# Kernel optimization log

Measured on AMD Instinct MI355X. Metric: run time of the kernel, lower is better.

The kernel has to match this reference:

```python
import jax, jax.numpy as jnp
import numpy as np
from jax import lax

N_QUBITS = 4
DIM = 2 ** N_QUBITS  # 16, amplitude-embedding feature size == clayer_in output
N_QLAYERS = 1
INPUT_SIZE = 128
HIDDEN_SIZE = 128
BATCH = 128
SEQ = 1024


def _cnot_perm(n):
    # Composed permutation matrix of the ansatz CNOT ladder:
    # for i in 1..2: for j in range(n): CNOT(wire j -> wire (j+i) % n)
    # PennyLane wire ordering: wire 0 is the most significant bit.
    dim = 2 ** n
    gates = []
    for i in range(1, 3):
        for j in range(n):
            gates.append((j, (j + i) % n))
    P = np.eye(dim, dtype=np.float32)
    for (c, t) in gates:
        cbit, tbit = n - 1 - c, n - 1 - t
        g = np.zeros((dim, dim), dtype=np.float32)
        for s in range(dim):
            s2 = s ^ (1 << tbit) if (s >> cbit) & 1 else s
            g[s2, s] = 1.0
        P = g @ P  # psi_new = P @ psi
    return P

_P = jnp.asarray(_cnot_perm(N_QUBITS))
# Z[s, w] = <s| PauliZ(wire w) |s>
_Z = jnp.asarray(np.array([[1.0 - 2.0 * ((s >> (N_QUBITS - 1 - w)) & 1)
                            for w in range(N_QUBITS)] for s in range(DIM)],
                           dtype=np.float32))


def _rx_kron(theta):
    # kron of per-wire RX(theta_i) gates, wire 0 most significant
    c = jnp.cos(theta / 2).astype(jnp.complex64)
    s = (-1j * jnp.sin(theta / 2)).astype(jnp.complex64)
    u = None
    for i in range(N_QUBITS):
        m = jnp.stack([jnp.stack([c[i], s[i]]), jnp.stack([s[i], c[i]])])
        u = m if u is None else jnp.kron(u, m)
    return u  # (DIM, DIM) complex64


def _vqc(y, weights):
    # AmplitudeEmbedding(normalize=True) + n_qlayers x (CNOT ladder, RX layer)
    # then expval(PauliZ) on each wire. y: (B, DIM) real, weights: (L, V, n)
    norm = jnp.sqrt(jnp.sum(y * y, axis=1, keepdims=True))
    psi = (y / norm).astype(jnp.complex64)  # (B, DIM)
    for l in range(N_QLAYERS):
        psi = psi @ _P.T               # CNOT ladder (permutation)
        psi = psi @ _rx_kron(weights[l, 0]).T  # RX layer (only vrotation 0 used)
    probs = (psi * jnp.conj(psi)).real
    return probs @ _Z  # (B, n_qubits)


def _cell(h, x_t, w_r, w_r1, w_u, W_in, b_in, W_out, b_out):
    y = jnp.concatenate([h, x_t], axis=1) @ W_in + b_in
    r = jax.nn.sigmoid(_vqc(y, w_r) @ W_out + b_out)
    v1 = jnp.concatenate([r * h, x_t], axis=1) @ W_in + b_in
    h2 = jnp.tanh(_vqc(v1, w_r1) @ W_out + b_out)
    z = jax.nn.sigmoid(_vqc(y, w_u) @ W_out + b_out)
    return (1.0 - z) * h + z * h2


def _run(xs, w_r, w_r1, w_u, W_in, b_in, W_out, b_out):
    # xs: (T, B, F); returns hidden states in loop order, shape (B, T, H)
    h0 = jnp.zeros((xs.shape[1], HIDDEN_SIZE), dtype=xs.dtype)
    def step(h, x_t):
        hn = _cell(h, x_t, w_r, w_r1, w_u, W_in, b_in, W_out, b_out)
        return hn, hn
    _, hs = lax.scan(step, h0, xs)
    return jnp.swapaxes(hs, 0, 1)


def setup_inputs() -> dict:
    key = jax.random.key(0)
    ks = jax.random.split(key, 11)
    concat = INPUT_SIZE + HIDDEN_SIZE
    two_pi = 2.0 * float(np.pi)
    return {
        "x": jax.random.normal(ks[0], (BATCH, SEQ, INPUT_SIZE), jnp.float32),
        "W_in": jax.random.normal(ks[1], (concat, DIM), jnp.float32) / np.float32(np.sqrt(concat)),
        "b_in": jax.random.normal(ks[2], (DIM,), jnp.float32) * 0.01,
        "W_out": jax.random.normal(ks[3], (N_QUBITS, HIDDEN_SIZE), jnp.float32) / np.float32(np.sqrt(N_QUBITS)),
        "b_out": jax.random.normal(ks[4], (HIDDEN_SIZE,), jnp.float32) * 0.01,
        "w_reset": jax.random.uniform(ks[5], (N_QLAYERS, 1, N_QUBITS), jnp.float32, 0.0, two_pi),
        "w_reset1": jax.random.uniform(ks[6], (N_QLAYERS, 1, N_QUBITS), jnp.float32, 0.0, two_pi),
        "w_update": jax.random.uniform(ks[7], (N_QLAYERS, 1, N_QUBITS), jnp.float32, 0.0, two_pi),
        "w_back_reset": jax.random.uniform(ks[8], (N_QLAYERS, 1, N_QUBITS), jnp.float32, 0.0, two_pi),
        "w_back_reset1": jax.random.uniform(ks[9], (N_QLAYERS, 1, N_QUBITS), jnp.float32, 0.0, two_pi),
        "w_back_update": jax.random.uniform(ks[10], (N_QLAYERS, 1, N_QUBITS), jnp.float32, 0.0, two_pi),
    }


def reference(x, W_in, b_in, W_out, b_out, w_reset, w_reset1, w_update,
              w_back_reset, w_back_reset1, w_back_update):
    xs = jnp.swapaxes(x, 0, 1)  # (T, B, F)
    fwd = _run(xs, w_reset, w_reset1, w_update, W_in, b_in, W_out, b_out)
    # Original backward loop iterates t = T-1..0 and stacks in loop order,
    # then adds WITHOUT flipping back. Reproduce that exactly.
    bwd = _run(xs[::-1], w_back_reset, w_back_reset1, w_back_update,
               W_in, b_in, W_out, b_out)
    return (fwd + bwd) / 2.0
```

## Files before the change

kernel.cpp:

```cpp
#include <hip/hip_runtime.h>
#include <hip/hip_bf16.h>

#define TSEQ 1024
#define NB   128
#define HID  128
#define QDIM 16

typedef unsigned int  u32;
typedef unsigned short u16;
typedef float f32x2 __attribute__((ext_vector_type(2)));


template<int CTRL>
__device__ __forceinline__ int dpp_i(int x) {
  return __builtin_amdgcn_update_dpp(0, x, CTRL, 0xF, 0xF, true);
}
template<int CTRL>
__device__ __forceinline__ float dpp_f(float x) {
  return __int_as_float(dpp_i<CTRL>(__float_as_int(x)));
}

#ifdef __has_builtin
#if __has_builtin(__builtin_amdgcn_permlane16_swap) && __has_builtin(__builtin_amdgcn_permlane32_swap)
#define HAS_PLS 1
#endif
#endif
#ifndef HAS_PLS
#define HAS_PLS 0
#endif

__device__ __forceinline__ float pls16_sum(float x) {
#if HAS_PLS
  auto r = __builtin_amdgcn_permlane16_swap(__float_as_uint(x), __float_as_uint(x), false, false);
  return __uint_as_float(r[0]) + __uint_as_float(r[1]);
#else
  return x + __shfl_xor(x, 16, 64);
#endif
}
__device__ __forceinline__ float pls32_sum(float x) {
#if HAS_PLS
  auto r = __builtin_amdgcn_permlane32_swap(__float_as_uint(x), __float_as_uint(x), false, false);
  return __uint_as_float(r[0]) + __uint_as_float(r[1]);
#else
  return x + __shfl_xor(x, 32, 64);
#endif
}

__device__ __forceinline__ float rcpf(float x) { return __builtin_amdgcn_rcpf(x); }

__device__ __forceinline__ float ex2(float x) {
#if defined(__has_builtin)
#if __has_builtin(__builtin_amdgcn_exp2f)
  return __builtin_amdgcn_exp2f(x);
#else
  return exp2f(x);
#endif
#else
  return exp2f(x);
#endif
}

__device__ __forceinline__ u16 f2bf(float f) {
  u32 u = __float_as_uint(f);
  u32 r = (u + 0x7FFFu + ((u >> 16) & 1u)) >> 16;
  return (u16)r;
}

__device__ __forceinline__ f32x2 s2(float x) { f32x2 r; r.x = x; r.y = x; return r; }

__device__ __forceinline__ int gperm(int t) {
  int u = t;
#define APPLY(c, tt) u ^= (((u >> (3 - (c))) & 1) << (3 - (tt)));
  APPLY(3, 1) APPLY(2, 0) APPLY(1, 3) APPLY(0, 2)
  APPLY(3, 0) APPLY(2, 3) APPLY(1, 2) APPLY(0, 1)
#undef APPLY
  return u;
}


__global__ __launch_bounds__(256) void xw_kernel(
    const float* __restrict__ x, const float* __restrict__ W_in,
    const float* __restrict__ b_in, float* __restrict__ xw) {
  __shared__ __align__(16) float xs[16][132];
  __shared__ float wl[2048];
  __shared__ float bl[16];
  const int tid = threadIdx.x;
  const long r0 = (long)blockIdx.x * 16;
#pragma unroll
  for (int i = 0; i < 8; ++i) {
    int idx = tid + i * 256;
    xs[idx >> 7][idx & 127] = x[(r0 + (idx >> 7)) * 128 + (idx & 127)];
  }
#pragma unroll
  for (int i = 0; i < 8; ++i) {
    int idx = tid + i * 256;
    wl[idx] = W_in[2048 + idx];
  }
  if (tid < 16) bl[tid] = b_in[tid];
  __syncthreads();
  const int rr = tid >> 4, j = tid & 15;
  const int gj = gperm(j);
  float s = bl[gj];
#pragma unroll
  for (int k4 = 0; k4 < 32; ++k4) {
    float4 v = *reinterpret_cast<const float4*>(&xs[rr][k4 * 4]);
    int kb = k4 * 4;
    s = fmaf(v.x, wl[(kb + 0) * 16 + gj], s);
    s = fmaf(v.y, wl[(kb + 1) * 16 + gj], s);
    s = fmaf(v.z, wl[(kb + 2) * 16 + gj], s);
    s = fmaf(v.w, wl[(kb + 3) * 16 + gj], s);
  }
  xw[(r0 + rr) * 16 + j] = s;
}


template<bool BF16WS>
__global__ __launch_bounds__(64)
__attribute__((amdgpu_waves_per_eu(1, 2)))
void qbigru_main(
    const float* __restrict__ W_in,
    const float* __restrict__ W_out,
    const float* __restrict__ b_out,
    const float* __restrict__ thr_f, const float* __restrict__ thr1_f, const float* __restrict__ thu_f,
    const float* __restrict__ thr_b, const float* __restrict__ thr1_b, const float* __restrict__ thu_b,
    const float* __restrict__ xw,
    float* __restrict__ out,
    void* __restrict__ bwdws) {
  const int tid = threadIdx.x;
  const int l4  = tid & 15;
  const int dir = blockIdx.x >> 7;
  const int b   = blockIdx.x & 127;

  const int pshl = dpp_i<0x104>(tid);
  const int sel4 = (pshl == (tid ^ 4)) ? ~0 : 0;
  auto xor4f = [&](float x) {
    int a = dpp_i<0x104>(__float_as_int(x));
    int c = dpp_i<0x114>(__float_as_int(x));
    return __int_as_float((a & sel4) | (c & ~sel4));
  };

  auto bfr = [&](const float* v) -> float {
    float w1[8];
#pragma unroll
    for (int j = 0; j < 8; ++j) w1[j] = v[2 * j] + dpp_f<0xB1>(v[2 * j + 1]);
    float w2[4];
#pragma unroll
    for (int j = 0; j < 4; ++j) w2[j] = w1[2 * j] + dpp_f<0x4E>(w1[2 * j + 1]);
    float w3[2];
#pragma unroll
    for (int j = 0; j < 2; ++j) w3[j] = w2[j] + dpp_f<0x128>(w2[j + 2]);
    float y0 = w3[0] + xor4f(w3[1]);
    return pls32_sum(pls16_sum(y0));
  };

  auto ebf = [&](float p, float& n2, float* eb) {
    float s4 = xor4f(p);
    float P  = p + s4, M2 = p - s4;
    float dP = dpp_f<0x128>(P), dM2 = dpp_f<0x128>(M2);
    float P3 = P + dP, M3 = P - dP; M2 = M2 + dM2;
    float a1 = dpp_f<0x4E>(P3), a2 = dpp_f<0x4E>(M3), a3 = dpp_f<0x4E>(M2);
    float P1 = P3 + a1, M1 = P3 - a1; M3 += a2; M2 += a3;
    float b0_ = dpp_f<0xB1>(P1), b1_ = dpp_f<0xB1>(M1), b3_ = dpp_f<0xB1>(M3), b2_ = dpp_f<0xB1>(M2);
    n2 = P1 + b0_;
    eb[0] = P1 - b0_; eb[1] = M1 + b1_; eb[3] = M3 + b3_; eb[2] = M2 + b2_;
  };

  const float* thr  = dir ? thr_b  : thr_f;
  const float* thr1 = dir ? thr1_b : thr1_f;
  const float* thu  = dir ? thu_b  : thu_f;

  const int k0 = 2 * tid, k1 = 2 * tid + 1;

  f32x2 w0p[8], w1p[8];
#pragma unroll
  for (int i = 0; i < 8; ++i) {
    int ja = gperm((2 * i) ^ l4), jb = gperm((2 * i + 1) ^ l4);
    f32x2 a, c;
    a.x = W_in[k0 * QDIM + ja];  a.y = W_in[k0 * QDIM + jb];
    c.x = W_in[k1 * QDIM + ja];  c.y = W_in[k1 * QDIM + jb];
    w0p[i] = a; w1p[i] = c;
  }

  const float L2E = 1.4426950408889634f;
  f32x2 woRpk[4], woZpk[4], woHpk[4];
#pragma unroll
  for (int B = 0; B < 4; ++B) {
    float sgn = ((tid >> B) & 1) ? -1.f : 1.f;
    float cR = cosf(thr[3 - B])  * sgn * (-L2E);
    float cZ = cosf(thu[3 - B])  * sgn * (-L2E);
    float cH = cosf(thr1[3 - B]) * sgn * (2.f * L2E);
    float wo0 = W_out[(3 - B) * HID + k0];
    float wo1 = W_out[(3 - B) * HID + k1];
    f32x2 rr_, zz_, hh_;
    rr_.x = wo0 * cR;  rr_.y = wo1 * cR;
    zz_.x = wo0 * cZ;  zz_.y = wo1 * cZ;
    hh_.x = wo0 * cH;  hh_.y = wo1 * cH;
    woRpk[B] = rr_; woZpk[B] = zz_; woHpk[B] = hh_;
  }
  f32x2 nbcpk, bc2pk;
  nbcpk.x = -b_out[k0] * L2E;         nbcpk.y = -b_out[k1] * L2E;
  bc2pk.x =  b_out[k0] * (2.f * L2E); bc2pk.y =  b_out[k1] * (2.f * L2E);

  auto dot4pk = [](const float* e, const f32x2* w) -> f32x2 {
    f32x2 d01 = s2(e[1]) * w[1] + s2(e[0]) * w[0];
    f32x2 d23 = s2(e[3]) * w[3] + s2(e[2]) * w[2];
    return d01 + d23;
  };

  f32x2 hpk; hpk.x = 0.f; hpk.y = 0.f;
  const float* pxw = xw + ((long)b * TSEQ + (dir ? TSEQ - 1 : 0)) * QDIM;
  const long xstep = dir ? -QDIM : QDIM;
  float xc = pxw[l4]; pxw += xstep;
  float xn = pxw[l4]; pxw += xstep;

  float* po  = out + (long)b * TSEQ * HID + k0;
  float* pbf = (float*)bwdws + (long)b * TSEQ * HID + k0;
  u32*   pbh = (u32*)bwdws + ((long)b * TSEQ * HID >> 1) + tid;

#pragma unroll 1
  for (int t = 0; t < TSEQ; ++t) {
    float xnn = pxw[l4]; pxw += xstep;

    f32x2 hh0 = s2(hpk.x);
    f32x2 hh1 = s2(hpk.y);
    float v[16];
#pragma unroll
    for (int i = 0; i < 8; ++i) {
      f32x2 a = hh0 * w0p[i] + hh1 * w1p[i];
      v[2 * i] = a.x; v[2 * i + 1] = a.y;
    }
    float yv = bfr(v) + xc;

    float prb = yv * yv;

    float n2, eb[4];
    ebf(prb, n2, eb);
    float inv = rcpf(n2);

    f32x2 rd = dot4pk(eb, woRpk);
    f32x2 zd = dot4pk(eb, woZpk);

    f32x2 ra = rd * s2(inv) + nbcpk;
    f32x2 za = zd * s2(inv) + nbcpk;
    float r0 = rcpf(1.f + ex2(ra.x));
    float r1 = rcpf(1.f + ex2(ra.y));
    float z0 = rcpf(1.f + ex2(za.x));
    float z1 = rcpf(1.f + ex2(za.y));

    f32x2 zpk;  zpk.x = z0; zpk.y = z1;
    f32x2 omz = s2(1.f) - zpk;
    f32x2 qpk = omz * hpk + zpk;
    f32x2 spk = s2(-2.f) * zpk;

    f32x2 rpk; rpk.x = r0; rpk.y = r1;
    f32x2 rh = rpk * hpk;
    hh0 = s2(rh.x);
    hh1 = s2(rh.y);
#pragma unroll
    for (int i = 0; i < 8; ++i) {
      f32x2 a = hh0 * w0p[i] + hh1 * w1p[i];
      v[2 * i] = a.x; v[2 * i + 1] = a.y;
    }
    float vv = bfr(v) + xc;

    float prb2 = vv * vv;

    float n2b, eb2[4];
    ebf(prb2, n2b, eb2);
    float invb = rcpf(n2b);
    f32x2 hd = dot4pk(eb2, woHpk);
    f32x2 ha = hd * s2(invb) + bc2pk;
    float wq0 = rcpf(1.f + ex2(ha.x));
    float wq1 = rcpf(1.f + ex2(ha.y));
    f32x2 wpk; wpk.x = wq0; wpk.y = wq1;
    hpk = spk * wpk + qpk;

    f32x2 opk = hpk * s2(0.5f);
    if (dir == 0) {
      *reinterpret_cast<f32x2*>(po) = opk;
      po += HID;
    } else if (BF16WS) {
      *pbh = (u32)f2bf(opk.x) | ((u32)f2bf(opk.y) << 16);
      pbh += HID / 2;
    } else {
      *reinterpret_cast<f32x2*>(pbf) = opk;
      pbf += HID;
    }

    xc = xn; xn = xnn;
  }
}


template<bool BF16WS>
__global__ __launch_bounds__(256) void combine_k(float* __restrict__ out,
                                                 const void* __restrict__ bwd, long n4) {
  long i = (long)blockIdx.x * 256 + threadIdx.x;
  const long stride = (long)gridDim.x * 256;
  for (; i < n4; i += stride) {
    float4 o = reinterpret_cast<float4*>(out)[i];
    float ax, ay, az, aw;
    if (BF16WS) {
      ushort4 u = reinterpret_cast<const ushort4*>(bwd)[i];
      ax = __uint_as_float((u32)u.x << 16);
      ay = __uint_as_float((u32)u.y << 16);
      az = __uint_as_float((u32)u.z << 16);
      aw = __uint_as_float((u32)u.w << 16);
    } else {
      float4 a = reinterpret_cast<const float4*>(bwd)[i];
      ax = a.x; ay = a.y; az = a.z; aw = a.w;
    }
    o.x += ax; o.y += ay; o.z += az; o.w += aw;
    reinterpret_cast<float4*>(out)[i] = o;
  }
}


extern "C" void kernel_launch(void* const* d_in, const int* in_sizes, int n_in,
                              void* d_out, int out_size, void* d_ws, size_t ws_size,
                              hipStream_t stream) {
  const float* x     = (const float*)d_in[0];
  const float* W_in  = (const float*)d_in[1];
  const float* b_in  = (const float*)d_in[2];
  const float* W_out = (const float*)d_in[3];
  const float* b_out = (const float*)d_in[4];
  const float* thr_f  = (const float*)d_in[5];
  const float* thr1_f = (const float*)d_in[6];
  const float* thu_f  = (const float*)d_in[7];
  const float* thr_b  = (const float*)d_in[8];
  const float* thr1_b = (const float*)d_in[9];
  const float* thu_b  = (const float*)d_in[10];
  float* out = (float*)d_out;

  char* ws = (char*)d_ws;
  const size_t PAD = 4096;
  const size_t xw_bytes = (size_t)NB * TSEQ * QDIM * sizeof(float);
  float* xw = (float*)(ws + PAD);
  void* bwd = (void*)(ws + PAD + xw_bytes + PAD);
  const size_t need_f32 = 2 * PAD + xw_bytes + (size_t)NB * TSEQ * HID * sizeof(float);
  const bool f32ws = (ws_size >= need_f32);

  xw_kernel<<<(NB * TSEQ) / 16, 256, 0, stream>>>(x, W_in, b_in, xw);

  if (f32ws) {
    qbigru_main<false><<<256, 64, 0, stream>>>(W_in, W_out, b_out,
        thr_f, thr1_f, thu_f, thr_b, thr1_b, thu_b, xw, out, bwd);
  } else {
    qbigru_main<true><<<256, 64, 0, stream>>>(W_in, W_out, b_out,
        thr_f, thr1_f, thu_f, thr_b, thr1_b, thu_b, xw, out, bwd);
  }

  const long n4 = (long)NB * TSEQ * HID / 4;
  if (f32ws) combine_k<false><<<2048, 256, 0, stream>>>(out, bwd, n4);
  else       combine_k<true><<<2048, 256, 0, stream>>>(out, bwd, n4);
}
```

Before: 590.8 us.

## Use row-rotate DPP butterfly reduction and always store backward output as bf16

Reworks the per-step 16-lane reduction to use DPP row-rotate patterns instead of xor swizzles, rotating the W_in weight assignment so each lane's partial products line up. A runtime probe of the rotate direction selects a specialized loop body. This removes the emulated xor-4 exchange (two DPP ops plus select) from the latency-critical recurrence. It also drops the fp32 backward workspace path and always writes bf16, halving workspace traffic at the cost of precision.

```diff
diff --git a/kernel.cpp b/kernel.cpp
--- a/kernel.cpp
+++ b/kernel.cpp
@@ -1,5 +1,6 @@
 #include <hip/hip_runtime.h>
 #include <hip/hip_bf16.h>
+#include <type_traits>
 
 #define TSEQ 1024
 #define NB   128
@@ -114,7 +115,6 @@
 }
 
 
-template<bool BF16WS>
 __global__ __launch_bounds__(64)
 __attribute__((amdgpu_waves_per_eu(1, 2)))
 void qbigru_main(
@@ -139,19 +139,8 @@
     return __int_as_float((a & sel4) | (c & ~sel4));
   };
 
-  auto bfr = [&](const float* v) -> float {
-    float w1[8];
-#pragma unroll
-    for (int j = 0; j < 8; ++j) w1[j] = v[2 * j] + dpp_f<0xB1>(v[2 * j + 1]);
-    float w2[4];
-#pragma unroll
-    for (int j = 0; j < 4; ++j) w2[j] = w1[2 * j] + dpp_f<0x4E>(w1[2 * j + 1]);
-    float w3[2];
-#pragma unroll
-    for (int j = 0; j < 2; ++j) w3[j] = w2[j] + dpp_f<0x128>(w2[j + 2]);
-    float y0 = w3[0] + xor4f(w3[1]);
-    return pls32_sum(pls16_sum(y0));
-  };
+  const int q1 = dpp_i<0x121>(l4);
+  const bool dplus = (q1 == ((l4 + 1) & 15));
 
   auto ebf = [&](float p, float& n2, float* eb) {
     float s4 = xor4f(p);
@@ -174,7 +163,7 @@
   f32x2 w0p[8], w1p[8];
 #pragma unroll
   for (int i = 0; i < 8; ++i) {
-    int ja = gperm((2 * i) ^ l4), jb = gperm((2 * i + 1) ^ l4);
+    int ja = gperm((2 * i + l4) & 15), jb = gperm((2 * i + 1 + l4) & 15);
     f32x2 a, c;
     a.x = W_in[k0 * QDIM + ja];  a.y = W_in[k0 * QDIM + jb];
     c.x = W_in[k1 * QDIM + ja];  c.y = W_in[k1 * QDIM + jb];
@@ -207,110 +196,122 @@
     return d01 + d23;
   };
 
-  f32x2 hpk; hpk.x = 0.f; hpk.y = 0.f;
-  const float* pxw = xw + ((long)b * TSEQ + (dir ? TSEQ - 1 : 0)) * QDIM;
-  const long xstep = dir ? -QDIM : QDIM;
-  float xc = pxw[l4]; pxw += xstep;
-  float xn = pxw[l4]; pxw += xstep;
-
-  float* po  = out + (long)b * TSEQ * HID + k0;
-  float* pbf = (float*)bwdws + (long)b * TSEQ * HID + k0;
-  u32*   pbh = (u32*)bwdws + ((long)b * TSEQ * HID >> 1) + tid;
+  auto body = [&](auto dpc) {
+    constexpr bool DP = decltype(dpc)::value;
+    constexpr int C2 = DP ? 0x12C : 0x124;
+    constexpr int C3 = DP ? 0x12E : 0x122;
+    constexpr int C4 = DP ? 0x12F : 0x121;
+
+    auto bfr = [&](const float* v) -> float {
+      float w1[8];
+#pragma unroll
+      for (int j = 0; j < 8; ++j) w1[j] = v[j] + dpp_f<0x128>(v[j + 8]);
+      float w2[4];
+#pragma unroll
+      for (int j = 0; j < 4; ++j) w2[j] = w1[j] + dpp_f<C2>(w1[j + 4]);
+      float w3[2];
+#pragma unroll
+      for (int j = 0; j < 2; ++j) w3[j] = w2[j] + dpp_f<C3>(w2[j + 2]);
+      float y0 = w3[0] + dpp_f<C4>(w3[1]);
+      return pls32_sum(pls16_sum(y0));
+    };
+
+    f32x2 hpk; hpk.x = 0.f; hpk.y = 0.f;
+    const float* pxw = xw + ((long)b * TSEQ + (dir ? TSEQ - 1 : 0)) * QDIM;
+    const long xstep = dir ? -QDIM : QDIM;
+    float xc = pxw[l4]; pxw += xstep;
+    float xn = pxw[l4]; pxw += xstep;
+
+    float* po  = out + (long)b * TSEQ * HID + k0;
+    u32*   pbh = (u32*)bwdws + ((long)b * TSEQ * HID >> 1) + tid;
 
 #pragma unroll 1
-  for (int t = 0; t < TSEQ; ++t) {
-    float xnn = pxw[l4]; pxw += xstep;
-
-    f32x2 hh0 = s2(hpk.x);
-    f32x2 hh1 = s2(hpk.y);
-    float v[16];
-#pragma unroll
-    for (int i = 0; i < 8; ++i) {
-      f32x2 a = hh0 * w0p[i] + hh1 * w1p[i];
-      v[2 * i] = a.x; v[2 * i + 1] = a.y;
+    for (int t = 0; t < TSEQ; ++t) {
+      float xnn = pxw[l4]; pxw += xstep;
+
+      f32x2 hh0 = s2(hpk.x);
+      f32x2 hh1 = s2(hpk.y);
+      float v[16];
+#pragma unroll
+      for (int i = 0; i < 8; ++i) {
+        f32x2 a = hh0 * w0p[i] + hh1 * w1p[i];
+        v[2 * i] = a.x; v[2 * i + 1] = a.y;
+      }
+      float yv = bfr(v) + xc;
+
+      float prb = yv * yv;
+
+      float n2, eb[4];
+      ebf(prb, n2, eb);
+      float inv = rcpf(n2);
+
+      f32x2 rd = dot4pk(eb, woRpk);
+      f32x2 zd = dot4pk(eb, woZpk);
+
+      f32x2 ra = rd * s2(inv) + nbcpk;
+      f32x2 za = zd * s2(inv) + nbcpk;
+      float r0 = rcpf(1.f + ex2(ra.x));
+      float r1 = rcpf(1.f + ex2(ra.y));
+      float z0 = rcpf(1.f + ex2(za.x));
+      float z1 = rcpf(1.f + ex2(za.y));
+
+      f32x2 zpk;  zpk.x = z0; zpk.y = z1;
+      f32x2 omz = s2(1.f) - zpk;
+      f32x2 qpk = omz * hpk + zpk;
+      f32x2 spk = s2(-2.f) * zpk;
+
+      f32x2 rpk; rpk.x = r0; rpk.y = r1;
+      f32x2 rh = rpk * hpk;
+      hh0 = s2(rh.x);
+      hh1 = s2(rh.y);
+#pragma unroll
+      for (int i = 0; i < 8; ++i) {
+        f32x2 a = hh0 * w0p[i] + hh1 * w1p[i];
+        v[2 * i] = a.x; v[2 * i + 1] = a.y;
+      }
+      float vv = bfr(v) + xc;
+
+      float prb2 = vv * vv;
+
+      float n2b, eb2[4];
+      ebf(prb2, n2b, eb2);
+      float invb = rcpf(n2b);
+      f32x2 hd = dot4pk(eb2, woHpk);
+      f32x2 ha = hd * s2(invb) + bc2pk;
+      float wq0 = rcpf(1.f + ex2(ha.x));
+      float wq1 = rcpf(1.f + ex2(ha.y));
+      f32x2 wpk; wpk.x = wq0; wpk.y = wq1;
+      hpk = spk * wpk + qpk;
+
+      f32x2 opk = hpk * s2(0.5f);
+      if (dir == 0) {
+        *reinterpret_cast<f32x2*>(po) = opk;
+        po += HID;
+      } else {
+        *pbh = (u32)f2bf(opk.x) | ((u32)f2bf(opk.y) << 16);
+        pbh += HID / 2;
+      }
+
+      xc = xn; xn = xnn;
     }
-    float yv = bfr(v) + xc;
-
-    float prb = yv * yv;
-
-    float n2, eb[4];
-    ebf(prb, n2, eb);
-    float inv = rcpf(n2);
-
-    f32x2 rd = dot4pk(eb, woRpk);
-    f32x2 zd = dot4pk(eb, woZpk);
-
-    f32x2 ra = rd * s2(inv) + nbcpk;
-    f32x2 za = zd * s2(inv) + nbcpk;
-    float r0 = rcpf(1.f + ex2(ra.x));
-    float r1 = rcpf(1.f + ex2(ra.y));
-    float z0 = rcpf(1.f + ex2(za.x));
-    float z1 = rcpf(1.f + ex2(za.y));
-
-    f32x2 zpk;  zpk.x = z0; zpk.y = z1;
-    f32x2 omz = s2(1.f) - zpk;
-    f32x2 qpk = omz * hpk + zpk;
-    f32x2 spk = s2(-2.f) * zpk;
-
-    f32x2 rpk; rpk.x = r0; rpk.y = r1;
-    f32x2 rh = rpk * hpk;
-    hh0 = s2(rh.x);
-    hh1 = s2(rh.y);
-#pragma unroll
-    for (int i = 0; i < 8; ++i) {
-      f32x2 a = hh0 * w0p[i] + hh1 * w1p[i];
-      v[2 * i] = a.x; v[2 * i + 1] = a.y;
-    }
-    float vv = bfr(v) + xc;
-
-    float prb2 = vv * vv;
-
-    float n2b, eb2[4];
-    ebf(prb2, n2b, eb2);
-    float invb = rcpf(n2b);
-    f32x2 hd = dot4pk(eb2, woHpk);
-    f32x2 ha = hd * s2(invb) + bc2pk;
-    float wq0 = rcpf(1.f + ex2(ha.x));
-    float wq1 = rcpf(1.f + ex2(ha.y));
-    f32x2 wpk; wpk.x = wq0; wpk.y = wq1;
-    hpk = spk * wpk + qpk;
-
-    f32x2 opk = hpk * s2(0.5f);
-    if (dir == 0) {
-      *reinterpret_cast<f32x2*>(po) = opk;
-      po += HID;
-    } else if (BF16WS) {
-      *pbh = (u32)f2bf(opk.x) | ((u32)f2bf(opk.y) << 16);
-      pbh += HID / 2;
-    } else {
-      *reinterpret_cast<f32x2*>(pbf) = opk;
-      pbf += HID;
-    }
-
-    xc = xn; xn = xnn;
-  }
-}
-
-
-template<bool BF16WS>
+  };
+
+  if (dplus) body(std::integral_constant<bool, true>{});
+  else       body(std::integral_constant<bool, false>{});
+}
+
+
 __global__ __launch_bounds__(256) void combine_k(float* __restrict__ out,
                                                  const void* __restrict__ bwd, long n4) {
   long i = (long)blockIdx.x * 256 + threadIdx.x;
   const long stride = (long)gridDim.x * 256;
   for (; i < n4; i += stride) {
     float4 o = reinterpret_cast<float4*>(out)[i];
-    float ax, ay, az, aw;
-    if (BF16WS) {
-      ushort4 u = reinterpret_cast<const ushort4*>(bwd)[i];
-      ax = __uint_as_float((u32)u.x << 16);
-      ay = __uint_as_float((u32)u.y << 16);
-      az = __uint_as_float((u32)u.z << 16);
-      aw = __uint_as_float((u32)u.w << 16);
-    } else {
-      float4 a = reinterpret_cast<const float4*>(bwd)[i];
-      ax = a.x; ay = a.y; az = a.z; aw = a.w;
-    }
-    o.x += ax; o.y += ay; o.z += az; o.w += aw;
+    ushort4 u = reinterpret_cast<const ushort4*>(bwd)[i];
+    o.x += __uint_as_float((u32)u.x << 16);
+    o.y += __uint_as_float((u32)u.y << 16);
+    o.z += __uint_as_float((u32)u.z << 16);
+    o.w += __uint_as_float((u32)u.w << 16);
     reinterpret_cast<float4*>(out)[i] = o;
   }
 }
@@ -337,20 +338,12 @@
   const size_t xw_bytes = (size_t)NB * TSEQ * QDIM * sizeof(float);
   float* xw = (float*)(ws + PAD);
   void* bwd = (void*)(ws + PAD + xw_bytes + PAD);
-  const size_t need_f32 = 2 * PAD + xw_bytes + (size_t)NB * TSEQ * HID * sizeof(float);
-  const bool f32ws = (ws_size >= need_f32);
 
   xw_kernel<<<(NB * TSEQ) / 16, 256, 0, stream>>>(x, W_in, b_in, xw);
 
-  if (f32ws) {
-    qbigru_main<false><<<256, 64, 0, stream>>>(W_in, W_out, b_out,
-        thr_f, thr1_f, thu_f, thr_b, thr1_b, thu_b, xw, out, bwd);
-  } else {
-    qbigru_main<true><<<256, 64, 0, stream>>>(W_in, W_out, b_out,
-        thr_f, thr1_f, thu_f, thr_b, thr1_b, thu_b, xw, out, bwd);
-  }
+  qbigru_main<<<256, 64, 0, stream>>>(W_in, W_out, b_out,
+      thr_f, thr1_f, thu_f, thr_b, thr1_b, thu_b, xw, out, bwd);
 
   const long n4 = (long)NB * TSEQ * HID / 4;
-  if (f32ws) combine_k<false><<<2048, 256, 0, stream>>>(out, bwd, n4);
-  else       combine_k<true><<<2048, 256, 0, stream>>>(out, bwd, n4);
-}
+  combine_k<<<2048, 256, 0, stream>>>(out, bwd, n4);
+}
```

After: 480.1 us. 1.23x faster.
